# Kernel optimization log

Hardware: AMD Instinct MI355X
Metric: run time of the kernel (lower is better)

## Reference

```python
import jax, jax.numpy as jnp
import numpy as np

N_NODES = 50000
N_EDGES = 800000
IN_FEAT = 4
HIDDEN = 128
NUM_LAYERS = 3


def setup_inputs() -> dict:
    key = jax.random.key(0)
    ks = jax.random.split(key, 16)
    x = jax.random.normal(ks[0], (N_NODES, IN_FEAT), dtype=jnp.float32)
    edge_index = jax.random.randint(ks[1], (2, N_EDGES), 0, N_NODES, dtype=jnp.int64)

    def lin(k, fan_in, fan_out):
        bound = 1.0 / np.sqrt(fan_in)
        k1, k2 = jax.random.split(k)
        W = jax.random.uniform(k1, (fan_in, fan_out), minval=-bound, maxval=bound, dtype=jnp.float32)
        b = jax.random.uniform(k2, (fan_out,), minval=-bound, maxval=bound, dtype=jnp.float32)
        return W, b

    W_enc, b_enc = lin(ks[2], IN_FEAT, HIDDEN)
    W_g1, b_g1 = lin(ks[3], HIDDEN, HIDDEN)
    W_g2, b_g2 = lin(ks[4], HIDDEN, HIDDEN)
    W_g3, b_g3 = lin(ks[5], HIDDEN, HIDDEN)
    W_m1, b_m1 = lin(ks[6], 2 * HIDDEN, HIDDEN)
    W_m2, b_m2 = lin(ks[7], HIDDEN, 3)
    return {
        "x": x, "edge_index": edge_index,
        "W_enc": W_enc, "b_enc": b_enc,
        "W_g1": W_g1, "b_g1": b_g1,
        "W_g2": W_g2, "b_g2": b_g2,
        "W_g3": W_g3, "b_g3": b_g3,
        "W_m1": W_m1, "b_m1": b_m1,
        "W_m2": W_m2, "b_m2": b_m2,
    }


def _gcn_forward(x, edge_index, W_enc, b_enc, gcn_params, W_m1, b_m1, W_m2, b_m2):
    n = x.shape[0]
    # Node encoder (linear + ReLU) -> [N, H]
    h = jax.nn.relu(x @ W_enc + b_enc)

    # Add self-loops once (GCNConv default add_self_loops=True)
    src = jnp.concatenate([edge_index[0], jnp.arange(n, dtype=edge_index.dtype)])
    dst = jnp.concatenate([edge_index[1], jnp.arange(n, dtype=edge_index.dtype)])
    # Symmetric degree normalization: D^{-1/2} (A+I) D^{-1/2}
    deg = jax.ops.segment_sum(jnp.ones_like(dst, dtype=h.dtype), dst, num_segments=n)
    deg_inv_sqrt = jnp.where(deg > 0, jax.lax.rsqrt(jnp.maximum(deg, 1.0)), 0.0)
    norm = (deg_inv_sqrt[src] * deg_inv_sqrt[dst])[:, None]  # [E+N, 1]

    for (W, b) in gcn_params:
        m = (h @ W)[src] * norm                       # gather + scale messages
        h = jax.ops.segment_sum(m, dst, num_segments=n) + b
        h = jax.nn.relu(h)                            # dropout is identity at eval

    # Edge classifier: gather endpoints, concat, MLP -> [E, 3]
    ef = jnp.concatenate([h[edge_index[0]], h[edge_index[1]]], axis=-1)
    return jax.nn.relu(ef @ W_m1 + b_m1) @ W_m2 + b_m2


def reference(x, edge_index, W_enc, b_enc, W_g1, b_g1, W_g2, b_g2, W_g3, b_g3, W_m1, b_m1, W_m2, b_m2):
    gcn_params = [(W_g1, b_g1), (W_g2, b_g2), (W_g3, b_g3)]
    return _gcn_forward(x, edge_index, W_enc, b_enc, gcn_params, W_m1, b_m1, W_m2, b_m2)
```

## Files before the change

kernel.cpp:

```cpp
#include <hip/hip_runtime.h>
#include <hip/hip_bf16.h>

#define N_NODES 50000
#define N_EDGES 800000
#define HID 128
#define NBUCKET 1024
#define N_NODE_BLOCKS ((N_NODES + 255) / 256)

typedef __attribute__((ext_vector_type(8))) short bf16x8;
typedef __attribute__((ext_vector_type(4))) float f32x4;

__device__ __forceinline__ ushort f2bf(float f) {
    uint u = __float_as_uint(f);
    return (ushort)((u + 0x7FFFu + ((u >> 16) & 1u)) >> 16);
}
__device__ __forceinline__ float bf2f(ushort h) { return __uint_as_float(((uint)h) << 16); }

__global__ void k_count(const int* __restrict__ ei, int* cnt) {
    int e = blockIdx.x * blockDim.x + threadIdx.x;
    if (e < N_EDGES) atomicAdd(&cnt[ei[N_EDGES + e]], 1);
}

__global__ __launch_bounds__(256) void k_bhist(const int* __restrict__ cnt, int* gHist,
                                               int* __restrict__ blockBase) {
    __shared__ int lh[NBUCKET];
    int t = threadIdx.x;
    for (int d = t; d < NBUCKET; d += 256) lh[d] = 0;
    __syncthreads();
    int n = blockIdx.x * 256 + t;
    if (n < N_NODES) {
        int deg = min(cnt[n], NBUCKET - 1);
        atomicAdd(&lh[deg], 1);
    }
    __syncthreads();
    for (int d = t; d < NBUCKET; d += 256) {
        int c = lh[d];
        blockBase[blockIdx.x * NBUCKET + d] = c ? atomicAdd(&gHist[d], c) : 0;
    }
}

__global__ __launch_bounds__(NBUCKET) void k_prefix(const int* __restrict__ gHist,
                                                    int* __restrict__ histBase,
                                                    int* __restrict__ edgeBase,
                                                    int* __restrict__ rowStartP) {
    __shared__ int a[NBUCKET];
    __shared__ int b[NBUCKET];
    int t = threadIdx.x;
    int h = gHist[t];
    a[t] = h;
    b[t] = h * t;
    __syncthreads();
    for (int off = 1; off < NBUCKET; off <<= 1) {
        int av = (t >= off) ? a[t - off] : 0;
        int bv = (t >= off) ? b[t - off] : 0;
        __syncthreads();
        a[t] += av;
        b[t] += bv;
        __syncthreads();
    }
    histBase[t] = a[t] - h;
    edgeBase[t] = b[t] - h * t;
    if (t == 0) rowStartP[N_NODES] = N_EDGES;
}

__global__ __launch_bounds__(256) void k_rank(const int* __restrict__ cnt,
                                              const int* __restrict__ histBase,
                                              const int* __restrict__ edgeBase,
                                              const int* __restrict__ blockBase,
                                              int* __restrict__ rank,
                                              int* __restrict__ invRank,
                                              int* __restrict__ rowStartP,
                                              float* __restrict__ dinvP) {
    __shared__ int cur[NBUCKET];
    int t = threadIdx.x;
    for (int d = t; d < NBUCKET; d += 256) cur[d] = 0;
    __syncthreads();
    int n = blockIdx.x * 256 + t;
    if (n < N_NODES) {
        int deg = min(cnt[n], NBUCKET - 1);
        int slot = atomicAdd(&cur[deg], 1);
        int r = histBase[deg] + blockBase[blockIdx.x * NBUCKET + deg] + slot;
        rank[n] = r;
        invRank[r] = n;
        rowStartP[r] = edgeBase[deg] + (r - histBase[deg]) * deg;
        dinvP[r] = rsqrtf(1.0f + (float)deg);
    }
}

__global__ void k_fill(const int* __restrict__ ei, const int* __restrict__ rank,
                       const int* __restrict__ rowStartP, int* cursorP,
                       int2* __restrict__ csrE) {
    int e = blockIdx.x * blockDim.x + threadIdx.x;
    if (e < N_EDGES) {
        int s = ei[e];
        int d = ei[N_EDGES + e];
        int rd = rank[d];
        int pos = rowStartP[rd] + atomicAdd(&cursorP[rd], 1);
        csrE[pos] = make_int2(rank[s], e);
    }
}

struct WSplitArgs {
    const float* src[5];
    ushort* th[5];
    ushort* tl[5];
};

__global__ void k_tsplit5(WSplitArgs a) {
    int i = blockIdx.x * 256 + threadIdx.x;
    int which = i >> 14, r = i & 16383;
    int k = r >> 7, j = r & 127;
    float v = a.src[which][r];
    ushort hi = f2bf(v);
    a.th[which][j * 128 + k] = hi;
    a.tl[which][j * 128 + k] = f2bf(v - bf2f(hi));
}

__global__ __launch_bounds__(512, 8) void k_enc_gemm(
    const float* __restrict__ x, const float* __restrict__ Wenc,
    const float* __restrict__ benc, const int* __restrict__ invRank,
    const float* __restrict__ dinvP,
    const ushort* __restrict__ BTH, const ushort* __restrict__ BTL,
    float* __restrict__ out) {
    __shared__ uint AsH[16][68];
    __shared__ uint AsL[16][68];
    int tid = threadIdx.x;

    if (tid < 256) {
        int ln = tid >> 4, li = tid & 15;
        int r = blockIdx.x * 16 + ln;
        int n = invRank[r];
        float4 xv = *(const float4*)(x + (size_t)n * 4);
        int j0 = li * 8;
        uint uh[4], ul[4];
#pragma unroll
        for (int p = 0; p < 4; ++p) {
            ushort hs[2], ls[2];
#pragma unroll
            for (int q = 0; q < 2; ++q) {
                int j = j0 + p * 2 + q;
                float acc = benc[j];
                acc += xv.x * Wenc[0 * 128 + j];
                acc += xv.y * Wenc[1 * 128 + j];
                acc += xv.z * Wenc[2 * 128 + j];
                acc += xv.w * Wenc[3 * 128 + j];
                float v = fmaxf(acc, 0.f);
                hs[q] = f2bf(v);
                ls[q] = f2bf(v - bf2f(hs[q]));
            }
            uh[p] = (uint)hs[0] | ((uint)hs[1] << 16);
            ul[p] = (uint)ls[0] | ((uint)ls[1] << 16);
        }
        *(uint4*)&AsH[ln][li * 4] = make_uint4(uh[0], uh[1], uh[2], uh[3]);
        *(uint4*)&AsL[ln][li * 4] = make_uint4(ul[0], ul[1], ul[2], ul[3]);
    }
    __syncthreads();

    int w = tid >> 6, l = tid & 63;
    int ln = l & 15, lk = l >> 4;
    int ct = w;
    int node = blockIdx.x * 16 + ln;
    f32x4 acc = {};
#pragma unroll
    for (int kc = 0; kc < 4; ++kc) {
        uint4 uhv = *(uint4*)&AsH[ln][kc * 16 + lk * 4];
        uint4 ulv = *(uint4*)&AsL[ln][kc * 16 + lk * 4];
        bf16x8 hh, hl;
        __builtin_memcpy(&hh, &uhv, 16);
        __builtin_memcpy(&hl, &ulv, 16);
        size_t boff = (size_t)(ct * 16 + ln) * 128 + kc * 32 + lk * 8;
        bf16x8 wh = *(const bf16x8*)(BTH + boff);
        bf16x8 wl = *(const bf16x8*)(BTL + boff);
        acc = __builtin_amdgcn_mfma_f32_16x16x32_bf16(wh, hh, acc, 0, 0, 0);
        acc = __builtin_amdgcn_mfma_f32_16x16x32_bf16(wl, hh, acc, 0, 0, 0);
        acc = __builtin_amdgcn_mfma_f32_16x16x32_bf16(wh, hl, acc, 0, 0, 0);
    }
    int jb = ct * 16 + lk * 4;
    float s = dinvP[node];
    *(float4*)(out + (size_t)node * 128 + jb) =
        make_float4(acc[0] * s, acc[1] * s, acc[2] * s, acc[3] * s);
}

__global__ __launch_bounds__(512, 8) void k_agg_gemm(
    const float* __restrict__ hw, const float* __restrict__ bg,
    const float* __restrict__ dinvP, const int* __restrict__ rowStartP,
    const int2* __restrict__ csrE,
    const ushort* __restrict__ BTH1, const ushort* __restrict__ BTL1,
    const ushort* __restrict__ BTH2, const ushort* __restrict__ BTL2,
    float* __restrict__ out1, float* __restrict__ out2,
    const float* __restrict__ b1, const float* __restrict__ outScale) {
    __shared__ uint AsH[16][68];
    __shared__ uint AsL[16][68];
    int tid = threadIdx.x;
    int w = tid >> 6, l = tid & 63;
    int sub = l >> 5;
    int g2 = (l >> 4) & 1;
    int li = l & 15;
    int c8 = li * 8;
    int n = blockIdx.x * 16 + w * 2 + sub;

    float4 aA, aB;
    if (g2 == 0) {
        aA = *(const float4*)(hw + (size_t)n * 128 + c8);
        aB = *(const float4*)(hw + (size_t)n * 128 + c8 + 4);
    } else {
        aA = make_float4(0.f, 0.f, 0.f, 0.f);
        aB = aA;
    }
    int s0 = rowStartP[n], s1 = rowStartP[n + 1];
    int k = s0 + g2;
    float4 v0a = make_float4(0.f, 0.f, 0.f, 0.f), v0b = v0a;
    if (k < s1) {
        const float* r = hw + (size_t)csrE[k].x * 128 + c8;
        v0a = *(const float4*)(r);
        v0b = *(const float4*)(r + 4);
    }
    for (; k < s1; k += 2) {
        float4 v1a = make_float4(0.f, 0.f, 0.f, 0.f), v1b = v1a;
        if (k + 2 < s1) {
            const float* r = hw + (size_t)csrE[k + 2].x * 128 + c8;
            v1a = *(const float4*)(r);
            v1b = *(const float4*)(r + 4);
        }
        aA.x += v0a.x; aA.y += v0a.y; aA.z += v0a.z; aA.w += v0a.w;
        aB.x += v0b.x; aB.y += v0b.y; aB.z += v0b.z; aB.w += v0b.w;
        v0a = v1a;
        v0b = v1b;
    }
    aA.x += __shfl_xor(aA.x, 16); aA.y += __shfl_xor(aA.y, 16);
    aA.z += __shfl_xor(aA.z, 16); aA.w += __shfl_xor(aA.w, 16);
    aB.x += __shfl_xor(aB.x, 16); aB.y += __shfl_xor(aB.y, 16);
    aB.z += __shfl_xor(aB.z, 16); aB.w += __shfl_xor(aB.w, 16);

    if (g2 == 0) {
        float di = dinvP[n];
        float4 bbA = *(const float4*)(bg + c8);
        float4 bbB = *(const float4*)(bg + c8 + 4);
        float f0 = fmaxf(bbA.x + di * aA.x, 0.f);
        float f1 = fmaxf(bbA.y + di * aA.y, 0.f);
        float f2 = fmaxf(bbA.z + di * aA.z, 0.f);
        float f3 = fmaxf(bbA.w + di * aA.w, 0.f);
        float f4 = fmaxf(bbB.x + di * aB.x, 0.f);
        float f5 = fmaxf(bbB.y + di * aB.y, 0.f);
        float f6 = fmaxf(bbB.z + di * aB.z, 0.f);
        float f7 = fmaxf(bbB.w + di * aB.w, 0.f);
        ushort h0 = f2bf(f0), h1 = f2bf(f1), h2 = f2bf(f2), h3 = f2bf(f3);
        ushort h4 = f2bf(f4), h5 = f2bf(f5), h6 = f2bf(f6), h7 = f2bf(f7);
        uint4 uh = make_uint4((uint)h0 | ((uint)h1 << 16), (uint)h2 | ((uint)h3 << 16),
                              (uint)h4 | ((uint)h5 << 16), (uint)h6 | ((uint)h7 << 16));
        ushort l0 = f2bf(f0 - bf2f(h0)), l1 = f2bf(f1 - bf2f(h1));
        ushort l2 = f2bf(f2 - bf2f(h2)), l3 = f2bf(f3 - bf2f(h3));
        ushort l4 = f2bf(f4 - bf2f(h4)), l5 = f2bf(f5 - bf2f(h5));
        ushort l6 = f2bf(f6 - bf2f(h6)), l7 = f2bf(f7 - bf2f(h7));
        uint4 ul = make_uint4((uint)l0 | ((uint)l1 << 16), (uint)l2 | ((uint)l3 << 16),
                              (uint)l4 | ((uint)l5 << 16), (uint)l6 | ((uint)l7 << 16));
        int r = w * 2 + sub;
        *(uint4*)&AsH[r][li * 4] = uh;
        *(uint4*)&AsL[r][li * 4] = ul;
    }
    __syncthreads();

    int ln = l & 15, lk = l >> 4;
    int ct = w;
    int node = blockIdx.x * 16 + ln;
    f32x4 acc1 = {};
    f32x4 acc2 = {};
#pragma unroll
    for (int kc = 0; kc < 4; ++kc) {
        uint4 uh = *(uint4*)&AsH[ln][kc * 16 + lk * 4];
        uint4 ul = *(uint4*)&AsL[ln][kc * 16 + lk * 4];
        bf16x8 hh, hl;
        __builtin_memcpy(&hh, &uh, 16);
        __builtin_memcpy(&hl, &ul, 16);
        size_t boff = (size_t)(ct * 16 + ln) * 128 + kc * 32 + lk * 8;
        bf16x8 wh = *(const bf16x8*)(BTH1 + boff);
        bf16x8 wl = *(const bf16x8*)(BTL1 + boff);
        acc1 = __builtin_amdgcn_mfma_f32_16x16x32_bf16(wh, hh, acc1, 0, 0, 0);
        acc1 = __builtin_amdgcn_mfma_f32_16x16x32_bf16(wl, hh, acc1, 0, 0, 0);
        acc1 = __builtin_amdgcn_mfma_f32_16x16x32_bf16(wh, hl, acc1, 0, 0, 0);
        if (BTH2) {
            bf16x8 wh2 = *(const bf16x8*)(BTH2 + boff);
            bf16x8 wl2 = *(const bf16x8*)(BTL2 + boff);
            acc2 = __builtin_amdgcn_mfma_f32_16x16x32_bf16(wh2, hh, acc2, 0, 0, 0);
            acc2 = __builtin_amdgcn_mfma_f32_16x16x32_bf16(wl2, hh, acc2, 0, 0, 0);
            acc2 = __builtin_amdgcn_mfma_f32_16x16x32_bf16(wh2, hl, acc2, 0, 0, 0);
        }
    }
    int jb = ct * 16 + lk * 4;
    if (outScale) {
        float s = outScale[node];
        *(float4*)(out1 + (size_t)node * 128 + jb) =
            make_float4(acc1[0] * s, acc1[1] * s, acc1[2] * s, acc1[3] * s);
    } else {
        *(float4*)(out1 + (size_t)node * 128 + jb) =
            make_float4(acc1[0], acc1[1], acc1[2], acc1[3]);
        float4 bv = *(const float4*)(b1 + jb);
        *(float4*)(out2 + (size_t)node * 128 + jb) =
            make_float4(acc2[0] + bv.x, acc2[1] + bv.y, acc2[2] + bv.z, acc2[3] + bv.w);
    }
}

__global__ __launch_bounds__(256) void k_edge_final(const float* __restrict__ P,
                                                    const float* __restrict__ Qb,
                                                    const int* __restrict__ rowStartP,
                                                    const int2* __restrict__ csrE,
                                                    const float* __restrict__ W2,
                                                    const float* __restrict__ b2,
                                                    float* __restrict__ out) {
    int wid = (blockIdx.x * 256 + threadIdx.x) >> 6;
    int l = threadIdx.x & 63;
    if (wid >= N_NODES) return;
    int s0 = rowStartP[wid], s1 = rowStartP[wid + 1];
    if (s0 >= s1) return;
    int j8 = (l & 15) * 8;
    int g = l >> 4;

    float4 qa = *(const float4*)(Qb + (size_t)wid * 128 + j8);
    float4 qb = *(const float4*)(Qb + (size_t)wid * 128 + j8 + 4);
    float w2r[8][3];
#pragma unroll
    for (int k = 0; k < 8; ++k) {
        w2r[k][0] = W2[(j8 + k) * 3 + 0];
        w2r[k][1] = W2[(j8 + k) * 3 + 1];
        w2r[k][2] = W2[(j8 + k) * 3 + 2];
    }
    float bz0 = b2[0], bz1 = b2[1], bz2 = b2[2];

    int k = s0 + g;
    int2 c = make_int2(0, 0);
    float4 pa = make_float4(0.f, 0.f, 0.f, 0.f), pb = pa;
    if (k < s1) {
        c = csrE[k];
        const float* pr = P + (size_t)c.x * 128 + j8;
        pa = *(const float4*)(pr);
        pb = *(const float4*)(pr + 4);
    }
    for (; k < s1; k += 4) {
        int kn = k + 4;
        int2 cn = make_int2(0, 0);
        float4 pan = make_float4(0.f, 0.f, 0.f, 0.f), pbn = pan;
        if (kn < s1) {
            cn = csrE[kn];
            const float* prn = P + (size_t)cn.x * 128 + j8;
            pan = *(const float4*)(prn);
            pbn = *(const float4*)(prn + 4);
        }
        float z[8];
        z[0] = fmaxf(pa.x + qa.x, 0.f);
        z[1] = fmaxf(pa.y + qa.y, 0.f);
        z[2] = fmaxf(pa.z + qa.z, 0.f);
        z[3] = fmaxf(pa.w + qa.w, 0.f);
        z[4] = fmaxf(pb.x + qb.x, 0.f);
        z[5] = fmaxf(pb.y + qb.y, 0.f);
        z[6] = fmaxf(pb.z + qb.z, 0.f);
        z[7] = fmaxf(pb.w + qb.w, 0.f);
        float o0 = 0.f, o1 = 0.f, o2 = 0.f;
#pragma unroll
        for (int q = 0; q < 8; ++q) {
            o0 += z[q] * w2r[q][0];
            o1 += z[q] * w2r[q][1];
            o2 += z[q] * w2r[q][2];
        }
#pragma unroll
        for (int m = 1; m < 16; m <<= 1) {
            o0 += __shfl_xor(o0, m);
            o1 += __shfl_xor(o1, m);
            o2 += __shfl_xor(o2, m);
        }
        if ((l & 15) == 0) {
            float* op = out + (size_t)c.y * 3;
            op[0] = o0 + bz0;
            op[1] = o1 + bz1;
            op[2] = o2 + bz2;
        }
        c = cn;
        pa = pan;
        pb = pbn;
    }
}

extern "C" void kernel_launch(void* const* d_in, const int* in_sizes, int n_in,
                              void* d_out, int out_size, void* d_ws, size_t ws_size,
                              hipStream_t stream) {
    const float* x     = (const float*)d_in[0];
    const int*   ei    = (const int*)d_in[1];
    const float* W_enc = (const float*)d_in[2];
    const float* b_enc = (const float*)d_in[3];
    const float* Wg[3] = {(const float*)d_in[4], (const float*)d_in[6], (const float*)d_in[8]};
    const float* bg[3] = {(const float*)d_in[5], (const float*)d_in[7], (const float*)d_in[9]};
    const float* W_m1  = (const float*)d_in[10];
    const float* b_m1  = (const float*)d_in[11];
    const float* W_m2  = (const float*)d_in[12];
    const float* b_m2  = (const float*)d_in[13];
    float* out = (float*)d_out;

    char* w = (char*)d_ws;
    ushort* hH      = (ushort*)w;  w += (size_t)N_NODES * HID * 2;
    ushort* hL      = (ushort*)w;  w += (size_t)N_NODES * HID * 2;
    float*  bufA    = (float*)w;   w += (size_t)N_NODES * HID * 4;
    float*  bufB    = (float*)w;   w += (size_t)N_NODES * HID * 4;
    int2*   csrE    = (int2*)w;    w += (size_t)N_EDGES * 8;
    int*    cnt     = (int*)w;     w += (size_t)N_NODES * 4;
    int*    cursorP = (int*)w;     w += (size_t)N_NODES * 4;
    int*    gHist   = (int*)w;     w += NBUCKET * 4;
    size_t  zeroBytes = (size_t)(N_NODES * 2 + NBUCKET) * 4;
    int*    rank    = (int*)w;     w += (size_t)N_NODES * 4;
    int*    invRank = (int*)w;     w += (size_t)N_NODES * 4;
    int*    rowStartP = (int*)w;   w += (size_t)(N_NODES + 4) * 4;
    float*  dinvP   = (float*)w;   w += (size_t)N_NODES * 4;
    int*    histBase = (int*)w;    w += NBUCKET * 4;
    int*    edgeBase = (int*)w;    w += NBUCKET * 4;
    int*    blockBase = (int*)w;   w += (size_t)N_NODE_BLOCKS * NBUCKET * 4;
    ushort* WgTH[3], *WgTL[3];
    for (int i = 0; i < 3; ++i) {
        WgTH[i] = (ushort*)w; w += 128 * 128 * 2;
        WgTL[i] = (ushort*)w; w += 128 * 128 * 2;
    }
    ushort* WtTH = (ushort*)w; w += 128 * 128 * 2;
    ushort* WtTL = (ushort*)w; w += 128 * 128 * 2;
    ushort* WbTH = (ushort*)w; w += 128 * 128 * 2;
    ushort* WbTL = (ushort*)w; w += 128 * 128 * 2;

    float* P  = (float*)hH;
    float* Qb = bufB;

    hipMemsetAsync(cnt, 0, zeroBytes, stream);
    k_count<<<(N_EDGES + 255) / 256, 256, 0, stream>>>(ei, cnt);
    k_bhist<<<N_NODE_BLOCKS, 256, 0, stream>>>(cnt, gHist, blockBase);
    k_prefix<<<1, NBUCKET, 0, stream>>>(gHist, histBase, edgeBase, rowStartP);
    k_rank<<<N_NODE_BLOCKS, 256, 0, stream>>>(cnt, histBase, edgeBase, blockBase,
                                              rank, invRank, rowStartP, dinvP);
    k_fill<<<(N_EDGES + 255) / 256, 256, 0, stream>>>(ei, rank, rowStartP, cursorP, csrE);

    WSplitArgs wa;
    wa.src[0] = Wg[0]; wa.th[0] = WgTH[0]; wa.tl[0] = WgTL[0];
    wa.src[1] = Wg[1]; wa.th[1] = WgTH[1]; wa.tl[1] = WgTL[1];
    wa.src[2] = Wg[2]; wa.th[2] = WgTH[2]; wa.tl[2] = WgTL[2];
    wa.src[3] = W_m1;             wa.th[3] = WtTH; wa.tl[3] = WtTL;
    wa.src[4] = W_m1 + 128 * 128; wa.th[4] = WbTH; wa.tl[4] = WbTL;
    k_tsplit5<<<5 * 16384 / 256, 256, 0, stream>>>(wa);

    const int fusedGrid = N_NODES / 16;
    k_enc_gemm<<<fusedGrid, 512, 0, stream>>>(x, W_enc, b_enc, invRank, dinvP,
                                              WgTH[0], WgTL[0], bufA);

    k_agg_gemm<<<fusedGrid, 512, 0, stream>>>(bufA, bg[0], dinvP, rowStartP, csrE,
                                              WgTH[1], WgTL[1], nullptr, nullptr,
                                              bufB, nullptr, nullptr, dinvP);
    k_agg_gemm<<<fusedGrid, 512, 0, stream>>>(bufB, bg[1], dinvP, rowStartP, csrE,
                                              WgTH[2], WgTL[2], nullptr, nullptr,
                                              bufA, nullptr, nullptr, dinvP);
    k_agg_gemm<<<fusedGrid, 512, 0, stream>>>(bufA, bg[2], dinvP, rowStartP, csrE,
                                              WtTH, WtTL, WbTH, WbTL,
                                              P, Qb, b_m1, nullptr);

    k_edge_final<<<(N_NODES * 64) / 256, 256, 0, stream>>>(P, Qb, rowStartP, csrE,
                                                           W_m2, b_m2, out);
}
```

Before: 452.6 us.

## Process 64 nodes per block in agg_gemm to reuse weight fragments

Each block of the fused aggregate+GEMM kernel now handles 64 nodes instead of 16. Each wave gathers four rows in sequence, and the MFMA stage loads every weight fragment once and applies it to four row tiles. This cuts global weight reloads by four times and reduces block count. The cost is less parallelism for the latency-bound gather, four times more shared memory, and higher register pressure, which may lower occupancy.

Result: no change. 444.7 us (-1.8%).

```diff
diff --git a/kernel.cpp b/kernel.cpp
--- a/kernel.cpp
+++ b/kernel.cpp
@@ -189,114 +189,125 @@
     const ushort* __restrict__ BTH2, const ushort* __restrict__ BTL2,
     float* __restrict__ out1, float* __restrict__ out2,
     const float* __restrict__ b1, const float* __restrict__ outScale) {
-    __shared__ uint AsH[16][68];
-    __shared__ uint AsL[16][68];
+    __shared__ uint AsH[64][68];
+    __shared__ uint AsL[64][68];
     int tid = threadIdx.x;
     int w = tid >> 6, l = tid & 63;
     int sub = l >> 5;
     int g2 = (l >> 4) & 1;
     int li = l & 15;
     int c8 = li * 8;
-    int n = blockIdx.x * 16 + w * 2 + sub;
-
-    float4 aA, aB;
-    if (g2 == 0) {
-        aA = *(const float4*)(hw + (size_t)n * 128 + c8);
-        aB = *(const float4*)(hw + (size_t)n * 128 + c8 + 4);
-    } else {
-        aA = make_float4(0.f, 0.f, 0.f, 0.f);
-        aB = aA;
-    }
-    int s0 = rowStartP[n], s1 = rowStartP[n + 1];
-    int k = s0 + g2;
-    float4 v0a = make_float4(0.f, 0.f, 0.f, 0.f), v0b = v0a;
-    if (k < s1) {
-        const float* r = hw + (size_t)csrE[k].x * 128 + c8;
-        v0a = *(const float4*)(r);
-        v0b = *(const float4*)(r + 4);
-    }
-    for (; k < s1; k += 2) {
-        float4 v1a = make_float4(0.f, 0.f, 0.f, 0.f), v1b = v1a;
-        if (k + 2 < s1) {
-            const float* r = hw + (size_t)csrE[k + 2].x * 128 + c8;
-            v1a = *(const float4*)(r);
-            v1b = *(const float4*)(r + 4);
-        }
-        aA.x += v0a.x; aA.y += v0a.y; aA.z += v0a.z; aA.w += v0a.w;
-        aB.x += v0b.x; aB.y += v0b.y; aB.z += v0b.z; aB.w += v0b.w;
-        v0a = v1a;
-        v0b = v1b;
-    }
-    aA.x += __shfl_xor(aA.x, 16); aA.y += __shfl_xor(aA.y, 16);
-    aA.z += __shfl_xor(aA.z, 16); aA.w += __shfl_xor(aA.w, 16);
-    aB.x += __shfl_xor(aB.x, 16); aB.y += __shfl_xor(aB.y, 16);
-    aB.z += __shfl_xor(aB.z, 16); aB.w += __shfl_xor(aB.w, 16);
-
-    if (g2 == 0) {
-        float di = dinvP[n];
-        float4 bbA = *(const float4*)(bg + c8);
-        float4 bbB = *(const float4*)(bg + c8 + 4);
-        float f0 = fmaxf(bbA.x + di * aA.x, 0.f);
-        float f1 = fmaxf(bbA.y + di * aA.y, 0.f);
-        float f2 = fmaxf(bbA.z + di * aA.z, 0.f);
-        float f3 = fmaxf(bbA.w + di * aA.w, 0.f);
-        float f4 = fmaxf(bbB.x + di * aB.x, 0.f);
-        float f5 = fmaxf(bbB.y + di * aB.y, 0.f);
-        float f6 = fmaxf(bbB.z + di * aB.z, 0.f);
-        float f7 = fmaxf(bbB.w + di * aB.w, 0.f);
-        ushort h0 = f2bf(f0), h1 = f2bf(f1), h2 = f2bf(f2), h3 = f2bf(f3);
-        ushort h4 = f2bf(f4), h5 = f2bf(f5), h6 = f2bf(f6), h7 = f2bf(f7);
-        uint4 uh = make_uint4((uint)h0 | ((uint)h1 << 16), (uint)h2 | ((uint)h3 << 16),
-                              (uint)h4 | ((uint)h5 << 16), (uint)h6 | ((uint)h7 << 16));
-        ushort l0 = f2bf(f0 - bf2f(h0)), l1 = f2bf(f1 - bf2f(h1));
-        ushort l2 = f2bf(f2 - bf2f(h2)), l3 = f2bf(f3 - bf2f(h3));
-        ushort l4 = f2bf(f4 - bf2f(h4)), l5 = f2bf(f5 - bf2f(h5));
-        ushort l6 = f2bf(f6 - bf2f(h6)), l7 = f2bf(f7 - bf2f(h7));
-        uint4 ul = make_uint4((uint)l0 | ((uint)l1 << 16), (uint)l2 | ((uint)l3 << 16),
-                              (uint)l4 | ((uint)l5 << 16), (uint)l6 | ((uint)l7 << 16));
-        int r = w * 2 + sub;
-        *(uint4*)&AsH[r][li * 4] = uh;
-        *(uint4*)&AsL[r][li * 4] = ul;
+
+#pragma unroll
+    for (int q = 0; q < 4; ++q) {
+        int r = w * 8 + sub * 4 + q;
+        int n = blockIdx.x * 64 + r;
+        if (n >= N_NODES) n = N_NODES - 1;
+        float4 aA, aB;
+        if (g2 == 0) {
+            aA = *(const float4*)(hw + (size_t)n * 128 + c8);
+            aB = *(const float4*)(hw + (size_t)n * 128 + c8 + 4);
+        } else {
+            aA = make_float4(0.f, 0.f, 0.f, 0.f);
+            aB = aA;
+        }
+        int s0 = rowStartP[n], s1 = rowStartP[n + 1];
+        int k = s0 + g2;
+        float4 v0a = make_float4(0.f, 0.f, 0.f, 0.f), v0b = v0a;
+        if (k < s1) {
+            const float* rp = hw + (size_t)csrE[k].x * 128 + c8;
+            v0a = *(const float4*)(rp);
+            v0b = *(const float4*)(rp + 4);
+        }
+        for (; k < s1; k += 2) {
+            float4 v1a = make_float4(0.f, 0.f, 0.f, 0.f), v1b = v1a;
+            if (k + 2 < s1) {
+                const float* rp = hw + (size_t)csrE[k + 2].x * 128 + c8;
+                v1a = *(const float4*)(rp);
+                v1b = *(const float4*)(rp + 4);
+            }
+            aA.x += v0a.x; aA.y += v0a.y; aA.z += v0a.z; aA.w += v0a.w;
+            aB.x += v0b.x; aB.y += v0b.y; aB.z += v0b.z; aB.w += v0b.w;
+            v0a = v1a;
+            v0b = v1b;
+        }
+        aA.x += __shfl_xor(aA.x, 16); aA.y += __shfl_xor(aA.y, 16);
+        aA.z += __shfl_xor(aA.z, 16); aA.w += __shfl_xor(aA.w, 16);
+        aB.x += __shfl_xor(aB.x, 16); aB.y += __shfl_xor(aB.y, 16);
+        aB.z += __shfl_xor(aB.z, 16); aB.w += __shfl_xor(aB.w, 16);
+
+        if (g2 == 0) {
+            float di = dinvP[n];
+            float4 bbA = *(const float4*)(bg + c8);
+            float4 bbB = *(const float4*)(bg + c8 + 4);
+            float f0 = fmaxf(bbA.x + di * aA.x, 0.f);
+            float f1 = fmaxf(bbA.y + di * aA.y, 0.f);
+            float f2 = fmaxf(bbA.z + di * aA.z, 0.f);
+            float f3 = fmaxf(bbA.w + di * aA.w, 0.f);
+            float f4 = fmaxf(bbB.x + di * aB.x, 0.f);
+            float f5 = fmaxf(bbB.y + di * aB.y, 0.f);
+            float f6 = fmaxf(bbB.z + di * aB.z, 0.f);
+            float f7 = fmaxf(bbB.w + di * aB.w, 0.f);
+            ushort h0 = f2bf(f0), h1 = f2bf(f1), h2 = f2bf(f2), h3 = f2bf(f3);
+            ushort h4 = f2bf(f4), h5 = f2bf(f5), h6 = f2bf(f6), h7 = f2bf(f7);
+            uint4 uh = make_uint4((uint)h0 | ((uint)h1 << 16), (uint)h2 | ((uint)h3 << 16),
+                                  (uint)h4 | ((uint)h5 << 16), (uint)h6 | ((uint)h7 << 16));
+            ushort l0 = f2bf(f0 - bf2f(h0)), l1 = f2bf(f1 - bf2f(h1));
+            ushort l2 = f2bf(f2 - bf2f(h2)), l3 = f2bf(f3 - bf2f(h3));
+            ushort l4 = f2bf(f4 - bf2f(h4)), l5 = f2bf(f5 - bf2f(h5));
+            ushort l6 = f2bf(f6 - bf2f(h6)), l7 = f2bf(f7 - bf2f(h7));
+            uint4 ul = make_uint4((uint)l0 | ((uint)l1 << 16), (uint)l2 | ((uint)l3 << 16),
+                                  (uint)l4 | ((uint)l5 << 16), (uint)l6 | ((uint)l7 << 16));
+            *(uint4*)&AsH[r][li * 4] = uh;
+            *(uint4*)&AsL[r][li * 4] = ul;
+        }
     }
     __syncthreads();
 
     int ln = l & 15, lk = l >> 4;
     int ct = w;
-    int node = blockIdx.x * 16 + ln;
-    f32x4 acc1 = {};
-    f32x4 acc2 = {};
-#pragma unroll
-    for (int kc = 0; kc < 4; ++kc) {
-        uint4 uh = *(uint4*)&AsH[ln][kc * 16 + lk * 4];
-        uint4 ul = *(uint4*)&AsL[ln][kc * 16 + lk * 4];
-        bf16x8 hh, hl;
-        __builtin_memcpy(&hh, &uh, 16);
-        __builtin_memcpy(&hl, &ul, 16);
-        size_t boff = (size_t)(ct * 16 + ln) * 128 + kc * 32 + lk * 8;
-        bf16x8 wh = *(const bf16x8*)(BTH1 + boff);
-        bf16x8 wl = *(const bf16x8*)(BTL1 + boff);
-        acc1 = __builtin_amdgcn_mfma_f32_16x16x32_bf16(wh, hh, acc1, 0, 0, 0);
-        acc1 = __builtin_amdgcn_mfma_f32_16x16x32_bf16(wl, hh, acc1, 0, 0, 0);
-        acc1 = __builtin_amdgcn_mfma_f32_16x16x32_bf16(wh, hl, acc1, 0, 0, 0);
-        if (BTH2) {
-            bf16x8 wh2 = *(const bf16x8*)(BTH2 + boff);
-            bf16x8 wl2 = *(const bf16x8*)(BTL2 + boff);
-            acc2 = __builtin_amdgcn_mfma_f32_16x16x32_bf16(wh2, hh, acc2, 0, 0, 0);
-            acc2 = __builtin_amdgcn_mfma_f32_16x16x32_bf16(wl2, hh, acc2, 0, 0, 0);
-            acc2 = __builtin_amdgcn_mfma_f32_16x16x32_bf16(wh2, hl, acc2, 0, 0, 0);
-        }
-    }
     int jb = ct * 16 + lk * 4;
-    if (outScale) {
-        float s = outScale[node];
-        *(float4*)(out1 + (size_t)node * 128 + jb) =
-            make_float4(acc1[0] * s, acc1[1] * s, acc1[2] * s, acc1[3] * s);
-    } else {
-        *(float4*)(out1 + (size_t)node * 128 + jb) =
-            make_float4(acc1[0], acc1[1], acc1[2], acc1[3]);
-        float4 bv = *(const float4*)(b1 + jb);
-        *(float4*)(out2 + (size_t)node * 128 + jb) =
-            make_float4(acc2[0] + bv.x, acc2[1] + bv.y, acc2[2] + bv.z, acc2[3] + bv.w);
+#pragma unroll 1
+    for (int set = 0; set < 2; ++set) {
+        if (set && !BTH2) break;
+        const ushort* TH = set ? BTH2 : BTH1;
+        const ushort* TL = set ? BTL2 : BTL1;
+        f32x4 acc[4] = {};
+#pragma unroll
+        for (int kc = 0; kc < 4; ++kc) {
+            size_t boff = (size_t)(ct * 16 + ln) * 128 + kc * 32 + lk * 8;
+            bf16x8 wh = *(const bf16x8*)(TH + boff);
+            bf16x8 wl = *(const bf16x8*)(TL + boff);
+#pragma unroll
+            for (int rt = 0; rt < 4; ++rt) {
+                uint4 uhv = *(uint4*)&AsH[rt * 16 + ln][kc * 16 + lk * 4];
+                uint4 ulv = *(uint4*)&AsL[rt * 16 + ln][kc * 16 + lk * 4];
+                bf16x8 hh, hl;
+                __builtin_memcpy(&hh, &uhv, 16);
+                __builtin_memcpy(&hl, &ulv, 16);
+                acc[rt] = __builtin_amdgcn_mfma_f32_16x16x32_bf16(wh, hh, acc[rt], 0, 0, 0);
+                acc[rt] = __builtin_amdgcn_mfma_f32_16x16x32_bf16(wl, hh, acc[rt], 0, 0, 0);
+                acc[rt] = __builtin_amdgcn_mfma_f32_16x16x32_bf16(wh, hl, acc[rt], 0, 0, 0);
+            }
+        }
+#pragma unroll
+        for (int rt = 0; rt < 4; ++rt) {
+            int node = blockIdx.x * 64 + rt * 16 + ln;
+            if (node >= N_NODES) continue;
+            if (outScale) {
+                float s = outScale[node];
+                *(float4*)(out1 + (size_t)node * 128 + jb) =
+                    make_float4(acc[rt][0] * s, acc[rt][1] * s, acc[rt][2] * s, acc[rt][3] * s);
+            } else if (set == 0) {
+                *(float4*)(out1 + (size_t)node * 128 + jb) =
+                    make_float4(acc[rt][0], acc[rt][1], acc[rt][2], acc[rt][3]);
+            } else {
+                float4 bv = *(const float4*)(b1 + jb);
+                *(float4*)(out2 + (size_t)node * 128 + jb) =
+                    make_float4(acc[rt][0] + bv.x, acc[rt][1] + bv.y,
+                                acc[rt][2] + bv.z, acc[rt][3] + bv.w);
+            }
+        }
     }
 }
 
@@ -440,10 +451,10 @@
     wa.src[4] = W_m1 + 128 * 128; wa.th[4] = WbTH; wa.tl[4] = WbTL;
     k_tsplit5<<<5 * 16384 / 256, 256, 0, stream>>>(wa);
 
-    const int fusedGrid = N_NODES / 16;
-    k_enc_gemm<<<fusedGrid, 512, 0, stream>>>(x, W_enc, b_enc, invRank, dinvP,
-                                              WgTH[0], WgTL[0], bufA);
-
+    k_enc_gemm<<<N_NODES / 16, 512, 0, stream>>>(x, W_enc, b_enc, invRank, dinvP,
+                                                 WgTH[0], WgTL[0], bufA);
+
+    const int fusedGrid = (N_NODES + 63) / 64;
     k_agg_gemm<<<fusedGrid, 512, 0, stream>>>(bufA, bg[0], dinvP, rowStartP, csrE,
                                               WgTH[1], WgTL[1], nullptr, nullptr,
                                               bufB, nullptr, nullptr, dinvP);
```
